# Optimization experiments

Measured on AMD Instinct MI355X. Metric: run time of the kernel, lower is better.

## Reference

```python
import jax, jax.numpy as jnp
import numpy as np

EPS = 1e-20

def setup_inputs() -> dict:
    key = jax.random.key(0)
    k1, k2, k3, k4, k5 = jax.random.split(key, 5)
    B, S, E, D = 8, 2048, 1024, 1024
    x = jax.random.normal(k1, (B, S, E), dtype=jnp.float32)
    mask = jax.random.randint(k2, (B, S, S), 0, 2, dtype=jnp.int32)
    scale = 1.0 / np.sqrt(E)
    Wq = jax.random.normal(k3, (E, D), dtype=jnp.float32) * scale
    Wk = jax.random.normal(k4, (E, D), dtype=jnp.float32) * scale
    Wv = jax.random.normal(k5, (E, D), dtype=jnp.float32) * scale
    return {"x": x, "mask": mask, "Wq": Wq, "Wk": Wk, "Wv": Wv}

def masked_softmax(scores, mask, axis=-1):
    # non-standard: multiply scores by mask BEFORE softmax, re-mask, renormalize
    w = jax.nn.softmax(scores * mask, axis=axis)
    w = w * mask
    return w / (w.sum(axis, keepdims=True) + EPS)

def reference(x, mask, Wq, Wk, Wv):
    D = Wq.shape[1]
    m = mask.astype(x.dtype)                       # [B,S,S]
    q = jnp.einsum('bse,ed->bsd', x, Wq)
    k = jnp.einsum('bse,ed->bsd', x, Wk)
    v = jnp.einsum('bse,ed->bsd', x, Wv)
    scores = jnp.einsum('bqd,bkd->bqk', q, k) / jnp.sqrt(jnp.asarray(D, x.dtype))
    attn = masked_softmax(scores, m, axis=-1)      # [B,S,S]
    return jnp.einsum('bqk,bkd->bqd', attn, v)
```

## Files before the change

### kernel.cpp

```cpp
#include <hip/hip_runtime.h>
#include <hip/hip_bf16.h>

#define S_LEN 2048
#define E_DIM 1024
#define D_DIM 1024

typedef __bf16 bf16x8 __attribute__((ext_vector_type(8)));
typedef __bf16 bf16x4 __attribute__((ext_vector_type(4)));
typedef float f32x4 __attribute__((ext_vector_type(4)));

__device__ __forceinline__ __bf16 f2bf(float f) {
    unsigned u = __builtin_bit_cast(unsigned, f);
    u += 0x7fffu + ((u >> 16) & 1u);
    unsigned short h = (unsigned short)(u >> 16);
    return __builtin_bit_cast(__bf16, h);
}

__device__ __forceinline__ int swz(int row, int b) {
    return row * 128 + (b ^ ((row & 7) << 4));
}

__device__ __forceinline__ void async_cp16(void* lds, const void* g) {
    __builtin_amdgcn_global_load_lds(
        (const __attribute__((address_space(1))) void*)g,
        (__attribute__((address_space(3))) void*)lds, 16, 0, 0);
}

__device__ __forceinline__ void stage_half(char* halfBase, const char* gRow0,
                                           size_t strideB, int tid)
{
    const int r  = tid >> 3;
    const int cb = (tid & 7) * 16;
    const int sc = cb ^ ((r & 7) << 4);
    #pragma unroll
    for (int i = 0; i < 2; ++i) {
        async_cp16(halfBase + i * 8192 + ((tid >> 6) << 10),
                   gRow0 + (size_t)(i * 64 + r) * strideB + sc);
    }
}

#define PEND(n) do { asm volatile("s_waitcnt vmcnt(" #n ")" ::: "memory"); \
                     __builtin_amdgcn_s_barrier(); } while (0)

template<int QM, int QN, bool LA, bool LB>
__device__ __forceinline__ void phase8(const char* lsA, const char* lsB,
    int wrr, int wcc, int rl, int lh,
    bf16x8 (&a)[4][2], bf16x8 (&b)[2][2], f32x4 (&acc)[4][4][2])
{
    if (LA) {
        #pragma unroll
        for (int mi = 0; mi < 4; ++mi)
            #pragma unroll
            for (int ks = 0; ks < 2; ++ks)
                a[mi][ks] = *reinterpret_cast<const bf16x8*>(
                    lsA + swz(QM*128 + wrr*64 + mi*16 + rl, ks*64 + lh*16));
    }
    if (LB) {
        #pragma unroll
        for (int ni = 0; ni < 2; ++ni)
            #pragma unroll
            for (int ks = 0; ks < 2; ++ks)
                b[ni][ks] = *reinterpret_cast<const bf16x8*>(
                    lsB + swz(QN*128 + wcc*32 + ni*16 + rl, ks*64 + lh*16));
    }
    __builtin_amdgcn_s_setprio(1);
    #pragma unroll
    for (int mi = 0; mi < 4; ++mi)
        #pragma unroll
        for (int ni = 0; ni < 2; ++ni)
            #pragma unroll
            for (int ks = 0; ks < 2; ++ks)
                acc[QM*2+QN][mi][ni] = __builtin_amdgcn_mfma_f32_16x16x32_bf16(
                    a[mi][ks], b[ni][ks], acc[QM*2+QN][mi][ni], 0, 0, 0);
    __builtin_amdgcn_s_setprio(0);
}

__device__ __forceinline__ void gemm256(const char* gA, const char* gB,
    size_t sA, size_t sB, int nt, char* ls, f32x4 (&acc)[4][4][2])
{
    const int tid = threadIdx.x, lane = tid & 63, wid = tid >> 6;
    const int wrr = wid >> 2, wcc = wid & 3;
    const int rl = lane & 15, lh = lane >> 4;
    char* bufA[2] = { ls,         ls + 65536 };
    char* bufB[2] = { ls + 32768, ls + 98304 };

    bf16x8 a[4][2];
    bf16x8 bb[2][2][2];

    stage_half(bufA[0] + 0,     gA,                      sA, tid);
    stage_half(bufB[0] + 0,     gB,                      sB, tid);
    stage_half(bufB[0] + 16384, gB + (size_t)128 * sB,   sB, tid);
    stage_half(bufA[0] + 16384, gA + (size_t)128 * sA,   sA, tid);
    PEND(0);

    for (int u = 0; u < nt - 1; ++u) {
        const char* cA = bufA[u & 1];
        const char* cB = bufB[u & 1];
        char* nA = bufA[(u + 1) & 1];
        char* nB = bufB[(u + 1) & 1];
        const char* gAn = gA + (size_t)(u + 1) * 128;
        const char* gBn = gB + (size_t)(u + 1) * 128;

        stage_half(nA + 0,     gAn,                    sA, tid);
        phase8<0,0,true ,true >(cA, cB, wrr, wcc, rl, lh, a, bb[0], acc);
        PEND(4);
        stage_half(nB + 0,     gBn,                    sB, tid);
        phase8<0,1,false,true >(cA, cB, wrr, wcc, rl, lh, a, bb[1], acc);
        PEND(4);
        stage_half(nB + 16384, gBn + (size_t)128 * sB, sB, tid);
        phase8<1,1,true ,false>(cA, cB, wrr, wcc, rl, lh, a, bb[1], acc);
        PEND(4);
        stage_half(nA + 16384, gAn + (size_t)128 * sA, sA, tid);
        phase8<1,0,false,false>(cA, cB, wrr, wcc, rl, lh, a, bb[0], acc);
        PEND(4);
    }
    {
        const char* cA = bufA[(nt - 1) & 1];
        const char* cB = bufB[(nt - 1) & 1];
        phase8<0,0,true ,true >(cA, cB, wrr, wcc, rl, lh, a, bb[0], acc);
        PEND(2);
        phase8<0,1,false,true >(cA, cB, wrr, wcc, rl, lh, a, bb[1], acc);
        PEND(0);
        phase8<1,1,true ,false>(cA, cB, wrr, wcc, rl, lh, a, bb[1], acc);
        phase8<1,0,false,false>(cA, cB, wrr, wcc, rl, lh, a, bb[0], acc);
    }
}


__global__ __launch_bounds__(256) void cvt_x_kernel(
    const float* __restrict__ X, __bf16* __restrict__ Xb)
{
    const int n8 = (8 * S_LEN * E_DIM) / 8;
    for (int i = blockIdx.x * 256 + threadIdx.x; i < n8; i += gridDim.x * 256) {
        const float* p = X + (size_t)i * 8;
        float4 a = *reinterpret_cast<const float4*>(p);
        float4 b = *reinterpret_cast<const float4*>(p + 4);
        bf16x8 h = { f2bf(a.x), f2bf(a.y), f2bf(a.z), f2bf(a.w),
                     f2bf(b.x), f2bf(b.y), f2bf(b.z), f2bf(b.w) };
        *reinterpret_cast<bf16x8*>(Xb + (size_t)i * 8) = h;
    }
}

__global__ __launch_bounds__(256) void wt_kernel(
    const float* __restrict__ Wq, const float* __restrict__ Wk, const float* __restrict__ Wv,
    __bf16* __restrict__ Wt)
{
    __shared__ float t[64][68];
    const int z = blockIdx.z;
    const float* W = (z == 0) ? Wq : (z == 1) ? Wk : Wv;
    const int d0 = blockIdx.x * 64, e0 = blockIdx.y * 64;
    const int tid = threadIdx.x;

    const int er = tid >> 4, dc = (tid & 15) * 4;
    #pragma unroll
    for (int p = 0; p < 4; ++p) {
        int e = p * 16 + er;
        float4 v = *reinterpret_cast<const float4*>(W + (size_t)(e0 + e) * D_DIM + d0 + dc);
        *reinterpret_cast<float4*>(&t[e][dc]) = v;
    }
    __syncthreads();

    const int dl = tid >> 3, ec = (tid & 7) * 8;
    __bf16* O = Wt + (size_t)z * E_DIM * D_DIM;
    #pragma unroll
    for (int p = 0; p < 2; ++p) {
        int d = p * 32 + dl;
        bf16x8 h;
        #pragma unroll
        for (int j = 0; j < 8; ++j) h[j] = f2bf(t[ec + j][d]);
        *reinterpret_cast<bf16x8*>(O + (size_t)(d0 + d) * E_DIM + e0 + ec) = h;
    }
}

__global__ __launch_bounds__(512, 2) void qkv_kernel(
    const __bf16* __restrict__ Xb, const __bf16* __restrict__ Wt,
    __bf16* __restrict__ Qb, __bf16* __restrict__ Kb, __bf16* __restrict__ Vt)
{
    __shared__ __align__(16) char ls[131072];
    const int bx = blockIdx.x, mt = blockIdx.y, z = blockIdx.z;
    const int m0 = mt * 256, n0 = bx * 256;

    f32x4 acc[4][4][2] = {};
    gemm256((const char*)Xb + (size_t)m0 * (E_DIM * 2),
            (const char*)(Wt + (size_t)z * E_DIM * D_DIM) + (size_t)n0 * (E_DIM * 2),
            E_DIM * 2, E_DIM * 2, E_DIM / 64, ls, acc);

    const int tid = threadIdx.x, lane = tid & 63, wid = tid >> 6;
    const int wrr = wid >> 2, wcc = wid & 3;
    const int rl = lane & 15, lh = lane >> 4;

    if (z < 2) {
        __bf16* O = (z == 0) ? Qb : Kb;
        #pragma unroll
        for (int q = 0; q < 4; ++q) {
            #pragma unroll
            for (int mi = 0; mi < 4; ++mi) {
                int row = m0 + (q >> 1)*128 + wrr*64 + mi*16 + lh*4;
                #pragma unroll
                for (int ni = 0; ni < 2; ++ni) {
                    int col = n0 + (q & 1)*128 + wcc*32 + ni*16 + rl;
                    #pragma unroll
                    for (int r = 0; r < 4; ++r)
                        O[(size_t)(row + r) * D_DIM + col] = f2bf(acc[q][mi][ni][r]);
                }
            }
        }
    } else {
        const int bz = m0 >> 11;
        const int srow = m0 & 2047;
        __bf16* O = Vt + (size_t)bz * D_DIM * S_LEN;
        #pragma unroll
        for (int q = 0; q < 4; ++q) {
            #pragma unroll
            for (int mi = 0; mi < 4; ++mi) {
                int row = srow + (q >> 1)*128 + wrr*64 + mi*16 + lh*4;
                #pragma unroll
                for (int ni = 0; ni < 2; ++ni) {
                    int col = n0 + (q & 1)*128 + wcc*32 + ni*16 + rl;
                    bf16x4 h = { f2bf(acc[q][mi][ni][0]), f2bf(acc[q][mi][ni][1]),
                                 f2bf(acc[q][mi][ni][2]), f2bf(acc[q][mi][ni][3]) };
                    *reinterpret_cast<bf16x4*>(O + (size_t)col * S_LEN + row) = h;
                }
            }
        }
    }
}

__global__ __launch_bounds__(512, 2) void qk_kernel(
    const __bf16* __restrict__ Qb, const __bf16* __restrict__ Kb,
    const int* __restrict__ mask, __bf16* __restrict__ P, float* __restrict__ rowsum)
{
    __shared__ __align__(16) char ls[131072];
    const int kt = blockIdx.x, qt = blockIdx.y, bz = blockIdx.z;
    const int q0 = qt * 256, k0 = kt * 256;

    f32x4 acc[4][4][2] = {};
    gemm256((const char*)(Qb + (size_t)bz * S_LEN * D_DIM) + (size_t)q0 * (D_DIM * 2),
            (const char*)(Kb + (size_t)bz * S_LEN * D_DIM) + (size_t)k0 * (D_DIM * 2),
            D_DIM * 2, D_DIM * 2, D_DIM / 64, ls, acc);

    const int tid = threadIdx.x, lane = tid & 63, wid = tid >> 6;
    const int wrr = wid >> 2, wcc = wid & 3;
    const int rl = lane & 15, lh = lane >> 4;

    float rs[2][4][4] = {};
    const size_t mbase = (size_t)bz * S_LEN * S_LEN;
    #pragma unroll
    for (int q = 0; q < 4; ++q) {
        #pragma unroll
        for (int mi = 0; mi < 4; ++mi) {
            int row = q0 + (q >> 1)*128 + wrr*64 + mi*16 + lh*4;
            #pragma unroll
            for (int ni = 0; ni < 2; ++ni) {
                int col = k0 + (q & 1)*128 + wcc*32 + ni*16 + rl;
                #pragma unroll
                for (int r = 0; r < 4; ++r) {
                    float s = acc[q][mi][ni][r] * 0.03125f;
                    int mk = mask[mbase + (size_t)(row + r) * S_LEN + col];
                    float pv = mk ? __expf(s) : 0.0f;
                    rs[q >> 1][mi][r] += pv;
                    P[mbase + (size_t)(row + r) * S_LEN + col] = f2bf(pv);
                }
            }
        }
    }
    #pragma unroll
    for (int h = 0; h < 2; ++h) {
        #pragma unroll
        for (int mi = 0; mi < 4; ++mi) {
            #pragma unroll
            for (int r = 0; r < 4; ++r) {
                float v = rs[h][mi][r];
                v += __shfl_xor(v, 1);
                v += __shfl_xor(v, 2);
                v += __shfl_xor(v, 4);
                v += __shfl_xor(v, 8);
                if (rl == 0)
                    atomicAdd(&rowsum[bz * S_LEN + q0 + h*128 + wrr*64 + mi*16 + lh*4 + r], v);
            }
        }
    }
}

__global__ __launch_bounds__(512, 2) void pv_kernel(
    const __bf16* __restrict__ P, const __bf16* __restrict__ Vt,
    const float* __restrict__ rowsum, float* __restrict__ out)
{
    __shared__ __align__(16) char ls[131072];
    const int dt = blockIdx.x, qt = blockIdx.y, bz = blockIdx.z;
    const int q0 = qt * 256, d0c = dt * 256;

    f32x4 acc[4][4][2] = {};
    gemm256((const char*)(P  + (size_t)bz * S_LEN * S_LEN) + (size_t)q0  * (S_LEN * 2),
            (const char*)(Vt + (size_t)bz * D_DIM * S_LEN) + (size_t)d0c * (S_LEN * 2),
            S_LEN * 2, S_LEN * 2, S_LEN / 64, ls, acc);

    const int tid = threadIdx.x, lane = tid & 63, wid = tid >> 6;
    const int wrr = wid >> 2, wcc = wid & 3;
    const int rl = lane & 15, lh = lane >> 4;

    float* Ob = out + (size_t)bz * S_LEN * D_DIM;
    #pragma unroll
    for (int q = 0; q < 4; ++q) {
        #pragma unroll
        for (int mi = 0; mi < 4; ++mi) {
            int row = q0 + (q >> 1)*128 + wrr*64 + mi*16 + lh*4;
            float inv[4];
            #pragma unroll
            for (int r = 0; r < 4; ++r)
                inv[r] = 1.0f / (rowsum[bz * S_LEN + row + r] + 1e-20f);
            #pragma unroll
            for (int ni = 0; ni < 2; ++ni) {
                int col = d0c + (q & 1)*128 + wcc*32 + ni*16 + rl;
                #pragma unroll
                for (int r = 0; r < 4; ++r)
                    Ob[(size_t)(row + r) * D_DIM + col] = acc[q][mi][ni][r] * inv[r];
            }
        }
    }
}

extern "C" void kernel_launch(void* const* d_in, const int* in_sizes, int n_in,
                              void* d_out, int out_size, void* d_ws, size_t ws_size,
                              hipStream_t stream) {
    const float* x    = (const float*)d_in[0];
    const int*   mask = (const int*)  d_in[1];
    const float* Wq   = (const float*)d_in[2];
    const float* Wk   = (const float*)d_in[3];
    const float* Wv   = (const float*)d_in[4];
    float* out = (float*)d_out;

    char* ws = (char*)d_ws;
    const size_t SZ_QKV = (size_t)8 * S_LEN * D_DIM * 2;
    const size_t SZ_P   = (size_t)8 * S_LEN * S_LEN * 2;
    __bf16* Qb = (__bf16*)(ws);
    __bf16* Kb = (__bf16*)(ws + SZ_QKV);
    __bf16* Vt = (__bf16*)(ws + 2 * SZ_QKV);
    char*   pbase = ws + 3 * SZ_QKV;
    __bf16* P  = (__bf16*)pbase;
    __bf16* Xb = (__bf16*)pbase;
    __bf16* Wt = (__bf16*)(pbase + (size_t)8 * S_LEN * E_DIM * 2);
    float* rowsum = (float*)(ws + 3 * SZ_QKV + SZ_P);
    const size_t need = 3 * SZ_QKV + SZ_P + (size_t)8 * S_LEN * 4;
    if (ws_size < need) return;

    hipMemsetAsync(rowsum, 0, (size_t)8 * S_LEN * 4, stream);
    cvt_x_kernel<<<2048, 256, 0, stream>>>(x, Xb);
    wt_kernel  <<<dim3(16, 16, 3), 256, 0, stream>>>(Wq, Wk, Wv, Wt);
    qkv_kernel <<<dim3(4, 64, 3), 512, 0, stream>>>(Xb, Wt, Qb, Kb, Vt);
    qk_kernel  <<<dim3(8, 8, 8),  512, 0, stream>>>(Qb, Kb, mask, P, rowsum);
    pv_kernel  <<<dim3(4, 8, 8),  512, 0, stream>>>(P, Vt, rowsum, out);
}
```

Measured before the change: 562.1 us.

## Restructure GEMM main loop into ping-pong MFMA regions with finer vmcnt waits

```diff
diff --git a/kernel.cpp b/kernel.cpp
--- a/kernel.cpp
+++ b/kernel.cpp
@@ -39,41 +39,50 @@
     }
 }
 
-#define PEND(n) do { asm volatile("s_waitcnt vmcnt(" #n ")" ::: "memory"); \
-                     __builtin_amdgcn_s_barrier(); } while (0)
-
-template<int QM, int QN, bool LA, bool LB>
-__device__ __forceinline__ void phase8(const char* lsA, const char* lsB,
-    int wrr, int wcc, int rl, int lh,
-    bf16x8 (&a)[4][2], bf16x8 (&b)[2][2], f32x4 (&acc)[4][4][2])
-{
-    if (LA) {
-        #pragma unroll
-        for (int mi = 0; mi < 4; ++mi)
-            #pragma unroll
-            for (int ks = 0; ks < 2; ++ks)
-                a[mi][ks] = *reinterpret_cast<const bf16x8*>(
-                    lsA + swz(QM*128 + wrr*64 + mi*16 + rl, ks*64 + lh*16));
-    }
-    if (LB) {
-        #pragma unroll
-        for (int ni = 0; ni < 2; ++ni)
-            #pragma unroll
-            for (int ks = 0; ks < 2; ++ks)
-                b[ni][ks] = *reinterpret_cast<const bf16x8*>(
-                    lsB + swz(QN*128 + wcc*32 + ni*16 + rl, ks*64 + lh*16));
-    }
-    __builtin_amdgcn_s_setprio(1);
+template<int H>
+__device__ __forceinline__ void loadA(const char* lsA, int wrr, int rl, int lh,
+                                      bf16x8 (&a)[4][2])
+{
     #pragma unroll
     for (int mi = 0; mi < 4; ++mi)
         #pragma unroll
-        for (int ni = 0; ni < 2; ++ni)
-            #pragma unroll
-            for (int ks = 0; ks < 2; ++ks)
-                acc[QM*2+QN][mi][ni] = __builtin_amdgcn_mfma_f32_16x16x32_bf16(
-                    a[mi][ks], b[ni][ks], acc[QM*2+QN][mi][ni], 0, 0, 0);
-    __builtin_amdgcn_s_setprio(0);
-}
+        for (int ks = 0; ks < 2; ++ks)
+            a[mi][ks] = *reinterpret_cast<const bf16x8*>(
+                lsA + swz(H*128 + wrr*64 + mi*16 + rl, ks*64 + lh*16));
+}
+template<int H>
+__device__ __forceinline__ void loadB(const char* lsB, int wcc, int rl, int lh,
+                                      bf16x8 (&b2)[2][2])
+{
+    #pragma unroll
+    for (int ni = 0; ni < 2; ++ni)
+        #pragma unroll
+        for (int ks = 0; ks < 2; ++ks)
+            b2[ni][ks] = *reinterpret_cast<const bf16x8*>(
+                lsB + swz(H*128 + wcc*32 + ni*16 + rl, ks*64 + lh*16));
+}
+
+#define MFMA_REGION(QM, QN, BSLOT)                                               \
+    do {                                                                         \
+        __builtin_amdgcn_s_barrier();                                            \
+        asm volatile("s_waitcnt lgkmcnt(0)" ::: "memory");                       \
+        __builtin_amdgcn_sched_barrier(0);                                       \
+        __builtin_amdgcn_s_setprio(1);                                           \
+        _Pragma("unroll")                                                        \
+        for (int mi = 0; mi < 4; ++mi)                                           \
+            _Pragma("unroll")                                                    \
+            for (int ni = 0; ni < 2; ++ni)                                       \
+                _Pragma("unroll")                                                \
+                for (int ks = 0; ks < 2; ++ks)                                   \
+                    acc[(QM)*2+(QN)][mi][ni] =                                   \
+                        __builtin_amdgcn_mfma_f32_16x16x32_bf16(                 \
+                            a[mi][ks], BSLOT[ni][ks],                            \
+                            acc[(QM)*2+(QN)][mi][ni], 0, 0, 0);                  \
+        __builtin_amdgcn_s_setprio(0);                                           \
+        __builtin_amdgcn_s_barrier();                                            \
+    } while (0)
+
+#define VMCNT(n) asm volatile("s_waitcnt vmcnt(" #n ")" ::: "memory")
 
 __device__ __forceinline__ void gemm256(const char* gA, const char* gB,
     size_t sA, size_t sB, int nt, char* ls, f32x4 (&acc)[4][4][2])
@@ -87,11 +96,12 @@
     bf16x8 a[4][2];
     bf16x8 bb[2][2][2];
 
-    stage_half(bufA[0] + 0,     gA,                      sA, tid);
-    stage_half(bufB[0] + 0,     gB,                      sB, tid);
-    stage_half(bufB[0] + 16384, gB + (size_t)128 * sB,   sB, tid);
-    stage_half(bufA[0] + 16384, gA + (size_t)128 * sA,   sA, tid);
-    PEND(0);
+    stage_half(bufA[0] + 0,     gA,                    sA, tid);
+    stage_half(bufB[0] + 0,     gB,                    sB, tid);
+    stage_half(bufB[0] + 16384, gB + (size_t)128 * sB, sB, tid);
+    stage_half(bufA[0] + 16384, gA + (size_t)128 * sA, sA, tid);
+    VMCNT(4);
+    __builtin_amdgcn_s_barrier();
 
     for (int u = 0; u < nt - 1; ++u) {
         const char* cA = bufA[u & 1];
@@ -101,28 +111,43 @@
         const char* gAn = gA + (size_t)(u + 1) * 128;
         const char* gBn = gB + (size_t)(u + 1) * 128;
 
-        stage_half(nA + 0,     gAn,                    sA, tid);
-        phase8<0,0,true ,true >(cA, cB, wrr, wcc, rl, lh, a, bb[0], acc);
-        PEND(4);
-        stage_half(nB + 0,     gBn,                    sB, tid);
-        phase8<0,1,false,true >(cA, cB, wrr, wcc, rl, lh, a, bb[1], acc);
-        PEND(4);
+        loadA<0>(cA, wrr, rl, lh, a);
+        loadB<0>(cB, wcc, rl, lh, bb[0]);
+        stage_half(nA + 0, gAn, sA, tid);
+        stage_half(nB + 0, gBn, sB, tid);
+        VMCNT(6);
+        MFMA_REGION(0, 0, bb[0]);
+
+        loadB<1>(cB, wcc, rl, lh, bb[1]);
         stage_half(nB + 16384, gBn + (size_t)128 * sB, sB, tid);
-        phase8<1,1,true ,false>(cA, cB, wrr, wcc, rl, lh, a, bb[1], acc);
-        PEND(4);
+        VMCNT(6);
+        MFMA_REGION(0, 1, bb[1]);
+
+        loadA<1>(cA, wrr, rl, lh, a);
         stage_half(nA + 16384, gAn + (size_t)128 * sA, sA, tid);
-        phase8<1,0,false,false>(cA, cB, wrr, wcc, rl, lh, a, bb[0], acc);
-        PEND(4);
-    }
+        MFMA_REGION(1, 1, bb[1]);
+
+        VMCNT(4);
+        MFMA_REGION(1, 0, bb[0]);
+    }
+
     {
         const char* cA = bufA[(nt - 1) & 1];
         const char* cB = bufB[(nt - 1) & 1];
-        phase8<0,0,true ,true >(cA, cB, wrr, wcc, rl, lh, a, bb[0], acc);
-        PEND(2);
-        phase8<0,1,false,true >(cA, cB, wrr, wcc, rl, lh, a, bb[1], acc);
-        PEND(0);
-        phase8<1,1,true ,false>(cA, cB, wrr, wcc, rl, lh, a, bb[1], acc);
-        phase8<1,0,false,false>(cA, cB, wrr, wcc, rl, lh, a, bb[0], acc);
+
+        loadA<0>(cA, wrr, rl, lh, a);
+        loadB<0>(cB, wcc, rl, lh, bb[0]);
+        VMCNT(2);
+        MFMA_REGION(0, 0, bb[0]);
+
+        loadB<1>(cB, wcc, rl, lh, bb[1]);
+        VMCNT(0);
+        MFMA_REGION(0, 1, bb[1]);
+
+        loadA<1>(cA, wrr, rl, lh, a);
+        MFMA_REGION(1, 1, bb[1]);
+
+        MFMA_REGION(1, 0, bb[0]);
     }
 }
 
```

Result: slower. 704.8 us (+25.4%).
